# Kernel tuning notes

Measured on AMD Instinct MI355X. Metric: run time of the kernel, lower is better.

## Reference

```python
import jax, jax.numpy as jnp
import numpy as np

HEADS = 8


def setup_inputs() -> dict:
    key = jax.random.key(0)
    k0, k1, k2, k3 = jax.random.split(key, 4)
    N, C_in, T = 4, 256, 2048
    C_kq, C_out = 512, 512
    x = jax.random.normal(k0, (N, C_in, T), dtype=jnp.float32)
    # Conv1d(kernel_size=1, bias=False) weights squeezed to (out, in)
    Wq = jax.random.normal(k1, (C_kq, C_in), dtype=jnp.float32) * 0.02
    Wk = jax.random.normal(k2, (C_kq, C_in), dtype=jnp.float32) * 0.02
    Wv = jax.random.normal(k3, (C_out, C_in), dtype=jnp.float32) * 0.02
    return {"x": x, "Wq": Wq, "Wk": Wk, "Wv": Wv}


def reference(x, Wq, Wk, Wv):
    N, C, T = x.shape
    H = HEADS
    C_kq = Wq.shape[0]
    C_out = Wv.shape[0]
    dk = C_kq // H
    dv = C_out // H
    # 1x1 conv == per-timestep linear projection
    q = jnp.einsum('oc,nct->not', Wq, x).reshape(N, H, dk, T)
    k = jnp.einsum('oc,nct->not', Wk, x).reshape(N, H, dk, T)
    v = jnp.einsum('oc,nct->not', Wv, x).reshape(N, H, dv, T)
    scale = 1.0 / np.sqrt(dk)
    # scores[n,h,tk,tq] = sum_d q[n,h,d,tq] * k[n,h,d,tk]
    scores = jnp.einsum('nhdq,nhdk->nhkq', q, k) * scale
    attn = jax.nn.softmax(scores, axis=2)  # softmax over key axis tk
    # out[n,h,d,tq] = sum_tk attn[n,h,tk,tq] * v[n,h,d,tk]
    out = jnp.einsum('nhkq,nhdk->nhdq', attn, v)
    return out.reshape(N, C_out, T)
```

## Files before the change

### kernel.cpp

```cpp
#include <hip/hip_runtime.h>
#include <stdint.h>

#define T_SEQ 2048
#define CIN 256
#define COUT 512
#define NHEAD 8
#define DH 64
#define LROW 72

typedef __bf16 bf16x8 __attribute__((ext_vector_type(8)));
typedef float f32x4 __attribute__((ext_vector_type(4)));
typedef float f32x16 __attribute__((ext_vector_type(16)));
typedef unsigned short u16x8 __attribute__((ext_vector_type(8)));
typedef unsigned u32x4 __attribute__((ext_vector_type(4)));

static __device__ __forceinline__ unsigned short bf16_rne(float f) {
  unsigned u = __builtin_bit_cast(unsigned, f);
  u += 0x7FFFu + ((u >> 16) & 1u);
  return (unsigned short)(u >> 16);
}

static __device__ __forceinline__ unsigned cvt_pk_bf16(float lo, float hi) {
  unsigned r;
  asm("v_cvt_pk_bf16_f32 %0, %1, %2" : "=v"(r) : "v"(lo), "v"(hi));
  return r;
}

static __device__ __forceinline__ void plswap(unsigned& a, unsigned& b) {
  auto rr = __builtin_amdgcn_permlane32_swap((int)a, (int)b, false, false);
  a = (unsigned)rr[0];
  b = (unsigned)rr[1];
}

static __device__ __forceinline__ bf16x8 ld_frag(const unsigned short* p) {
  u16x8 v = *(const u16x8*)p;
  return __builtin_bit_cast(bf16x8, v);
}

__global__ __launch_bounds__(256) void pack_w_k(const float* __restrict__ wq,
                                                const float* __restrict__ wk,
                                                const float* __restrict__ wv,
                                                unsigned short* __restrict__ wb) {
  int i = blockIdx.x * 256 + threadIdx.x;
  const float* src = (i < 131072) ? wq : (i < 262144) ? wk : wv;
  wb[i] = bf16_rne(src[i & 131071]);
}

__global__ __launch_bounds__(256) void pack_xT_k(const float* __restrict__ x,
                                                 unsigned short* __restrict__ xT) {
  __shared__ float tile[64][65];
  const int n = blockIdx.z, c0 = blockIdx.y * 64, t0 = blockIdx.x * 64;
  const int i = threadIdx.x;
  {
    const int cc = i >> 2, tch = (i & 3) * 16;
    const float* src = x + ((size_t)n * CIN + c0 + cc) * T_SEQ + t0 + tch;
    const float4* s4 = (const float4*)src;
#pragma unroll
    for (int q = 0; q < 4; ++q) {
      float4 v = s4[q];
      tile[cc][tch + q * 4 + 0] = v.x;
      tile[cc][tch + q * 4 + 1] = v.y;
      tile[cc][tch + q * 4 + 2] = v.z;
      tile[cc][tch + q * 4 + 3] = v.w;
    }
  }
  __syncthreads();
  {
    const int tt = i >> 2, cch = (i & 3) * 16;
    unsigned short* dst = xT + ((size_t)n * T_SEQ + t0 + tt) * CIN + c0 + cch;
    u16x8 w0, w1;
#pragma unroll
    for (int j = 0; j < 8; ++j) w0[j] = bf16_rne(tile[cch + j][tt]);
#pragma unroll
    for (int j = 0; j < 8; ++j) w1[j] = bf16_rne(tile[cch + 8 + j][tt]);
    *(u16x8*)dst = w0;
    *(u16x8*)(dst + 8) = w1;
  }
}

__global__ __launch_bounds__(256) void proj_k(const unsigned short* __restrict__ wb,
                                              const unsigned short* __restrict__ xT,
                                              unsigned short* __restrict__ qb,
                                              unsigned short* __restrict__ kb,
                                              unsigned short* __restrict__ vb) {
  __shared__ unsigned short vt_lds[64][136];
  const int z = blockIdx.z;
  const int n = z / 3, w = z % 3;
  const unsigned short* W = wb + (size_t)w * COUT * CIN;
  const unsigned short* X = xT + (size_t)n * T_SEQ * CIN;
  const int tid = threadIdx.x, wave = tid >> 6, lane = tid & 63;
  const int c = lane & 15, g = lane >> 4;
  const int o0 = blockIdx.x * 64;
  const int t0 = blockIdx.y * 128 + wave * 32;

  f32x4 acc[2][4];
  const f32x4 z4 = {0.f, 0.f, 0.f, 0.f};
#pragma unroll
  for (int mt = 0; mt < 2; ++mt)
#pragma unroll
    for (int no = 0; no < 4; ++no) acc[mt][no] = z4;

  for (int c0 = 0; c0 < CIN; c0 += 32) {
    bf16x8 a[2], b[4];
#pragma unroll
    for (int mt = 0; mt < 2; ++mt)
      a[mt] = ld_frag(X + (size_t)(t0 + mt * 16 + c) * CIN + c0 + g * 8);
#pragma unroll
    for (int no = 0; no < 4; ++no)
      b[no] = ld_frag(W + (size_t)(o0 + no * 16 + c) * CIN + c0 + g * 8);
#pragma unroll
    for (int mt = 0; mt < 2; ++mt)
#pragma unroll
      for (int no = 0; no < 4; ++no)
        acc[mt][no] = __builtin_amdgcn_mfma_f32_16x16x32_bf16(a[mt], b[no], acc[mt][no], 0, 0, 0);
  }

  const int h = o0 >> 6;
  const size_t base = ((size_t)(n * NHEAD + h)) * T_SEQ * DH;
  if (w == 2) {
#pragma unroll
    for (int mt = 0; mt < 2; ++mt)
#pragma unroll
      for (int no = 0; no < 4; ++no) {
        const int d = no * 16 + c;
        const int lt = (wave * 32) + mt * 16 + 4 * g;
#pragma unroll
        for (int pr = 0; pr < 2; ++pr) {
          const unsigned pw = (unsigned)bf16_rne(acc[mt][no][2 * pr]) |
                              ((unsigned)bf16_rne(acc[mt][no][2 * pr + 1]) << 16);
          *(unsigned*)&vt_lds[d][lt + 2 * pr] = pw;
        }
      }
    __syncthreads();
    const int row = tid >> 2, seg = tid & 3;
    unsigned short* dst = vb + base + (size_t)row * T_SEQ + blockIdx.y * 128 + seg * 32;
    const unsigned short* srcl = &vt_lds[row][seg * 32];
#pragma unroll
    for (int q = 0; q < 4; ++q) *(u16x8*)(dst + q * 8) = *(const u16x8*)(srcl + q * 8);
  } else {
    unsigned short* dst = (w == 0) ? qb : kb;
    const float scale = (w == 0) ? 0.18033688011112043f : 1.0f;
#pragma unroll
    for (int mt = 0; mt < 2; ++mt)
#pragma unroll
      for (int no = 0; no < 4; ++no)
#pragma unroll
        for (int r = 0; r < 4; ++r) {
          const int t = t0 + mt * 16 + 4 * g + r;
          const int d = no * 16 + c;
          dst[base + (size_t)t * DH + d] = bf16_rne(acc[mt][no][r] * scale);
        }
  }
}

__global__ __launch_bounds__(512) void attn_k(const unsigned short* __restrict__ qb,
                                              const unsigned short* __restrict__ kb,
                                              const unsigned short* __restrict__ vbt,
                                              float* __restrict__ outp) {
  __shared__ unsigned short Kl[2][2][64 * LROW];
  __shared__ unsigned short Vt[2][2][64 * LROW];

  const int bid = blockIdx.x;
  const int sid = (bid & 7) * 64 + (bid >> 3);
  const int tqt = sid & 15, nh = sid >> 4;

  const int tid = threadIdx.x;
  const int wave = tid >> 6, lane = tid & 63;
  const int half = wave >> 2;
  const int ln = lane & 31, hi = lane >> 5;
  const int tq0 = tqt * 128 + (wave & 3) * 32;
  const unsigned short* Q = qb + (size_t)nh * T_SEQ * DH;
  const unsigned short* K = kb + (size_t)nh * T_SEQ * DH;
  const unsigned short* V = vbt + (size_t)nh * T_SEQ * DH;

  bf16x8 qf[4];
#pragma unroll
  for (int dblk = 0; dblk < 4; ++dblk)
    qf[dblk] = ld_frag(Q + (size_t)(tq0 + ln) * DH + dblk * 16 + hi * 8);

  const f32x16 z16 = {0.f, 0.f, 0.f, 0.f, 0.f, 0.f, 0.f, 0.f,
                      0.f, 0.f, 0.f, 0.f, 0.f, 0.f, 0.f, 0.f};
  f32x16 oacc0 = z16, oacc1 = z16;
  float l_run = 0.f;

  const int ht = tid & 255;
  const int srow = ht & 63, sseg = ht >> 6;
  const unsigned short* kseg = K + (size_t)(half * 1024 + srow) * DH + sseg * 16;
  const unsigned short* vseg = V + (size_t)srow * T_SEQ + half * 1024 + sseg * 16;
  const int swoff = srow * LROW + sseg * 16;
  const int row0 = ln * LROW;
  const int row1 = (32 + ln) * LROW;
  const int hioff = hi * 8;

  unsigned short* krb = &Kl[half][0][0];
  unsigned short* kab = &Kl[half][1][0];
  unsigned short* vrb = &Vt[half][0][0];
  unsigned short* vab = &Vt[half][1][0];
  {
    u16x8 k0 = *(const u16x8*)kseg;
    u16x8 k1 = *(const u16x8*)(kseg + 8);
    u16x8 v0 = *(const u16x8*)vseg;
    u16x8 v1 = *(const u16x8*)(vseg + 8);
    *(u16x8*)&krb[swoff] = k0;
    *(u16x8*)&krb[swoff + 8] = k1;
    *(u16x8*)&vrb[swoff] = v0;
    *(u16x8*)&vrb[swoff + 8] = v1;
  }
  __syncthreads();

  const int NT2 = T_SEQ / 64 / 2;
  for (int t = 0; t < NT2; ++t) {
    const bool pre = (t + 1 < NT2);
    u16x8 kn0, kn1, vn0, vn1;
    if (pre) {
      const unsigned short* ks = kseg + (size_t)(t + 1) * (64 * DH);
      kn0 = *(const u16x8*)ks;
      kn1 = *(const u16x8*)(ks + 8);
      const unsigned short* vs = vseg + (size_t)(t + 1) * 64;
      vn0 = *(const u16x8*)vs;
      vn1 = *(const u16x8*)(vs + 8);
    }
    f32x16 sa0 = z16, sa1 = z16;
    __builtin_amdgcn_s_setprio(1);
#pragma unroll
    for (int dblk = 0; dblk < 4; ++dblk) {
      bf16x8 ka0 = ld_frag(krb + row0 + dblk * 16 + hioff);
      bf16x8 ka1 = ld_frag(krb + row1 + dblk * 16 + hioff);
      sa0 = __builtin_amdgcn_mfma_f32_32x32x16_bf16(ka0, qf[dblk], sa0, 0, 0, 0);
      sa1 = __builtin_amdgcn_mfma_f32_32x32x16_bf16(ka1, qf[dblk], sa1, 0, 0, 0);
    }
    __builtin_amdgcn_s_setprio(0);
    float p0[16], p1[16];
    float cs = 0.f;
#pragma unroll
    for (int r = 0; r < 16; ++r) {
      p0[r] = __builtin_amdgcn_exp2f(sa0[r]);
      p1[r] = __builtin_amdgcn_exp2f(sa1[r]);
      cs += p0[r] + p1[r];
    }
    cs += __shfl_xor(cs, 32);
    l_run += cs;
    unsigned W0[8], W1[8];
#pragma unroll
    for (int j = 0; j < 8; ++j) {
      W0[j] = cvt_pk_bf16(p0[2 * j], p0[2 * j + 1]);
      W1[j] = cvt_pk_bf16(p1[2 * j], p1[2 * j + 1]);
    }
    plswap(W0[0], W0[2]);
    plswap(W0[1], W0[3]);
    plswap(W0[4], W0[6]);
    plswap(W0[5], W0[7]);
    plswap(W1[0], W1[2]);
    plswap(W1[1], W1[3]);
    plswap(W1[4], W1[6]);
    plswap(W1[5], W1[7]);
    bf16x8 pa[4];
    {
      u32x4 f;
      f[0] = W0[0]; f[1] = W0[1]; f[2] = W0[2]; f[3] = W0[3];
      pa[0] = __builtin_bit_cast(bf16x8, f);
      f[0] = W0[4]; f[1] = W0[5]; f[2] = W0[6]; f[3] = W0[7];
      pa[1] = __builtin_bit_cast(bf16x8, f);
      f[0] = W1[0]; f[1] = W1[1]; f[2] = W1[2]; f[3] = W1[3];
      pa[2] = __builtin_bit_cast(bf16x8, f);
      f[0] = W1[4]; f[1] = W1[5]; f[2] = W1[6]; f[3] = W1[7];
      pa[3] = __builtin_bit_cast(bf16x8, f);
    }
    __builtin_amdgcn_s_setprio(1);
#pragma unroll
    for (int kbk = 0; kbk < 4; ++kbk) {
      bf16x8 vf0 = ld_frag(vrb + row0 + kbk * 16 + hioff);
      bf16x8 vf1 = ld_frag(vrb + row1 + kbk * 16 + hioff);
      oacc0 = __builtin_amdgcn_mfma_f32_32x32x16_bf16(pa[kbk], vf0, oacc0, 0, 0, 0);
      oacc1 = __builtin_amdgcn_mfma_f32_32x32x16_bf16(pa[kbk], vf1, oacc1, 0, 0, 0);
    }
    __builtin_amdgcn_s_setprio(0);
    if (pre) {
      *(u16x8*)&kab[swoff] = kn0;
      *(u16x8*)&kab[swoff + 8] = kn1;
      *(u16x8*)&vab[swoff] = vn0;
      *(u16x8*)&vab[swoff + 8] = vn1;
    }
    __syncthreads();
    unsigned short* tp;
    tp = krb; krb = kab; kab = tp;
    tp = vrb; vrb = vab; vab = tp;
  }

  float* mbuf = (float*)&Kl[0][0][0];
  const int MS = 2112;
  if (half == 1) {
    float* mb = mbuf + (wave - 4) * MS;
#pragma unroll
    for (int r = 0; r < 16; ++r) mb[r * 64 + lane] = oacc0[r];
#pragma unroll
    for (int r = 0; r < 16; ++r) mb[1024 + r * 64 + lane] = oacc1[r];
    mb[2048 + lane] = l_run;
  }
  __syncthreads();
  if (half == 0) {
    float* mb = mbuf + wave * MS;
#pragma unroll
    for (int r = 0; r < 16; ++r) oacc0[r] += mb[r * 64 + lane];
#pragma unroll
    for (int r = 0; r < 16; ++r) oacc1[r] += mb[1024 + r * 64 + lane];
    l_run += mb[2048 + lane];

    const int n = nh >> 3, h = nh & 7;
    const size_t obase = (size_t)(n * COUT + h * DH) * T_SEQ;
    const int d0 = ln, d1 = 32 + ln;
#pragma unroll
    for (int rq = 0; rq < 4; ++rq) {
      const int tbase = tq0 + 8 * rq + 4 * hi;
      f32x4 o0, o1;
#pragma unroll
      for (int j = 0; j < 4; ++j) {
        const float lv = __shfl(l_run, 8 * rq + 4 * hi + j);
        const float inv = __builtin_amdgcn_rcpf(lv);
        o0[j] = oacc0[4 * rq + j] * inv;
        o1[j] = oacc1[4 * rq + j] * inv;
      }
      *(f32x4*)&outp[obase + (size_t)d0 * T_SEQ + tbase] = o0;
      *(f32x4*)&outp[obase + (size_t)d1 * T_SEQ + tbase] = o1;
    }
  }
}

extern "C" void kernel_launch(void* const* d_in, const int* in_sizes, int n_in,
                              void* d_out, int out_size, void* d_ws, size_t ws_size,
                              hipStream_t stream) {
  (void)in_sizes; (void)n_in; (void)out_size; (void)ws_size;
  const float* x  = (const float*)d_in[0];
  const float* Wq = (const float*)d_in[1];
  const float* Wk = (const float*)d_in[2];
  const float* Wv = (const float*)d_in[3];
  float* outp = (float*)d_out;

  char* ws = (char*)d_ws;
  unsigned short* wb = (unsigned short*)ws;
  unsigned short* xT = (unsigned short*)(ws + 786432);
  unsigned short* qb = (unsigned short*)(ws + 4980736);
  unsigned short* kb = qb + 4194304;
  unsigned short* vb = kb + 4194304;

  pack_w_k<<<1536, 256, 0, stream>>>(Wq, Wk, Wv, wb);
  pack_xT_k<<<dim3(32, 4, 4), 256, 0, stream>>>(x, xT);
  proj_k<<<dim3(8, 16, 12), 256, 0, stream>>>(wb, xT, qb, kb, vb);
  attn_k<<<512, 512, 0, stream>>>(qb, kb, vb, outp);
}
```

Before: 105.5 us.

## Ping-pong QK and softmax/PV phases between the two wave halves

Splits each loop iteration into two barrier-separated phases and staggers the halves: while one half runs the QK MFMAs, the other runs exp/softmax and the PV MFMAs on the previous tile. Half 1's PV lags by one tile and is finished after the loop. The goal is to overlap the matrix-core work of one wave group with the transcendental/VALU work of the other. The cost is an extra __syncthreads per iteration and scores held in registers across the barrier, which may add register pressure.

```diff
diff --git a/kernel.cpp b/kernel.cpp
--- a/kernel.cpp
+++ b/kernel.cpp
@@ -192,50 +192,26 @@
   const int row1 = (32 + ln) * LROW;
   const int hioff = hi * 8;
 
-  unsigned short* krb = &Kl[half][0][0];
-  unsigned short* kab = &Kl[half][1][0];
-  unsigned short* vrb = &Vt[half][0][0];
-  unsigned short* vab = &Vt[half][1][0];
-  {
-    u16x8 k0 = *(const u16x8*)kseg;
-    u16x8 k1 = *(const u16x8*)(kseg + 8);
-    u16x8 v0 = *(const u16x8*)vseg;
-    u16x8 v1 = *(const u16x8*)(vseg + 8);
-    *(u16x8*)&krb[swoff] = k0;
-    *(u16x8*)&krb[swoff + 8] = k1;
-    *(u16x8*)&vrb[swoff] = v0;
-    *(u16x8*)&vrb[swoff + 8] = v1;
-  }
-  __syncthreads();
-
-  const int NT2 = T_SEQ / 64 / 2;
-  for (int t = 0; t < NT2; ++t) {
-    const bool pre = (t + 1 < NT2);
-    u16x8 kn0, kn1, vn0, vn1;
-    if (pre) {
-      const unsigned short* ks = kseg + (size_t)(t + 1) * (64 * DH);
-      kn0 = *(const u16x8*)ks;
-      kn1 = *(const u16x8*)(ks + 8);
-      const unsigned short* vs = vseg + (size_t)(t + 1) * 64;
-      vn0 = *(const u16x8*)vs;
-      vn1 = *(const u16x8*)(vs + 8);
-    }
-    f32x16 sa0 = z16, sa1 = z16;
+  auto qk = [&](const unsigned short* kbp, f32x16& s0, f32x16& s1) {
+    s0 = z16;
+    s1 = z16;
     __builtin_amdgcn_s_setprio(1);
 #pragma unroll
     for (int dblk = 0; dblk < 4; ++dblk) {
-      bf16x8 ka0 = ld_frag(krb + row0 + dblk * 16 + hioff);
-      bf16x8 ka1 = ld_frag(krb + row1 + dblk * 16 + hioff);
-      sa0 = __builtin_amdgcn_mfma_f32_32x32x16_bf16(ka0, qf[dblk], sa0, 0, 0, 0);
-      sa1 = __builtin_amdgcn_mfma_f32_32x32x16_bf16(ka1, qf[dblk], sa1, 0, 0, 0);
+      bf16x8 ka0 = ld_frag(kbp + row0 + dblk * 16 + hioff);
+      bf16x8 ka1 = ld_frag(kbp + row1 + dblk * 16 + hioff);
+      s0 = __builtin_amdgcn_mfma_f32_32x32x16_bf16(ka0, qf[dblk], s0, 0, 0, 0);
+      s1 = __builtin_amdgcn_mfma_f32_32x32x16_bf16(ka1, qf[dblk], s1, 0, 0, 0);
     }
     __builtin_amdgcn_s_setprio(0);
+  };
+  auto smpv = [&](const f32x16& s0, const f32x16& s1, const unsigned short* vbp) {
     float p0[16], p1[16];
     float cs = 0.f;
 #pragma unroll
     for (int r = 0; r < 16; ++r) {
-      p0[r] = __builtin_amdgcn_exp2f(sa0[r]);
-      p1[r] = __builtin_amdgcn_exp2f(sa1[r]);
+      p0[r] = __builtin_amdgcn_exp2f(s0[r]);
+      p1[r] = __builtin_amdgcn_exp2f(s1[r]);
       cs += p0[r] + p1[r];
     }
     cs += __shfl_xor(cs, 32);
@@ -269,12 +245,54 @@
     __builtin_amdgcn_s_setprio(1);
 #pragma unroll
     for (int kbk = 0; kbk < 4; ++kbk) {
-      bf16x8 vf0 = ld_frag(vrb + row0 + kbk * 16 + hioff);
-      bf16x8 vf1 = ld_frag(vrb + row1 + kbk * 16 + hioff);
+      bf16x8 vf0 = ld_frag(vbp + row0 + kbk * 16 + hioff);
+      bf16x8 vf1 = ld_frag(vbp + row1 + kbk * 16 + hioff);
       oacc0 = __builtin_amdgcn_mfma_f32_32x32x16_bf16(pa[kbk], vf0, oacc0, 0, 0, 0);
       oacc1 = __builtin_amdgcn_mfma_f32_32x32x16_bf16(pa[kbk], vf1, oacc1, 0, 0, 0);
     }
     __builtin_amdgcn_s_setprio(0);
+  };
+
+  unsigned short* krb = &Kl[half][0][0];
+  unsigned short* kab = &Kl[half][1][0];
+  unsigned short* vrb = &Vt[half][0][0];
+  unsigned short* vab = &Vt[half][1][0];
+  {
+    u16x8 k0 = *(const u16x8*)kseg;
+    u16x8 k1 = *(const u16x8*)(kseg + 8);
+    u16x8 v0 = *(const u16x8*)vseg;
+    u16x8 v1 = *(const u16x8*)(vseg + 8);
+    *(u16x8*)&krb[swoff] = k0;
+    *(u16x8*)&krb[swoff + 8] = k1;
+    *(u16x8*)&vrb[swoff] = v0;
+    *(u16x8*)&vrb[swoff + 8] = v1;
+  }
+  __syncthreads();
+
+  f32x16 sa0, sa1;
+  const int NT2 = T_SEQ / 64 / 2;
+  for (int t = 0; t < NT2; ++t) {
+    const bool pre = (t + 1 < NT2);
+    u16x8 kn0, kn1, vn0, vn1;
+    if (pre) {
+      const unsigned short* ks = kseg + (size_t)(t + 1) * (64 * DH);
+      kn0 = *(const u16x8*)ks;
+      kn1 = *(const u16x8*)(ks + 8);
+      const unsigned short* vs = vseg + (size_t)(t + 1) * 64;
+      vn0 = *(const u16x8*)vs;
+      vn1 = *(const u16x8*)(vs + 8);
+    }
+    if (half == 0) {
+      qk(krb, sa0, sa1);
+    } else if (t > 0) {
+      smpv(sa0, sa1, vab);
+    }
+    __syncthreads();
+    if (half == 0) {
+      smpv(sa0, sa1, vrb);
+    } else {
+      qk(krb, sa0, sa1);
+    }
     if (pre) {
       *(u16x8*)&kab[swoff] = kn0;
       *(u16x8*)&kab[swoff + 8] = kn1;
@@ -286,6 +304,7 @@
     tp = krb; krb = kab; kab = tp;
     tp = vrb; vrb = vab; vab = tp;
   }
+  if (half == 1) smpv(sa0, sa1, vab);
 
   float* mbuf = (float*)&Kl[0][0][0];
   const int MS = 2112;
```

Result: slower. 113.2 us (+7.3%).

## Fuse QKV projections per block and drop split-K attention for smaller blocks

Applied to the files above, without the earlier changes.

The projection kernel now loads the X fragments once into registers and loops over the three weight matrices (Q, K, V) inside one block, cutting grid z from 12 to 4 and reusing activations. The attention kernel drops the two-half key split and its LDS merge, using 128-thread blocks of 64 queries that walk all 32 key tiles, launched as 1024 blocks. This removes the cross-half reduction and halves LDS per block. In exchange each wave runs a longer serial key loop, and proj_k holds more registers for the cached fragments.

```diff
diff --git a/kernel.cpp b/kernel.cpp
--- a/kernel.cpp
+++ b/kernel.cpp
@@ -84,91 +84,97 @@
                                               unsigned short* __restrict__ kb,
                                               unsigned short* __restrict__ vb) {
   __shared__ unsigned short vt_lds[64][136];
-  const int z = blockIdx.z;
-  const int n = z / 3, w = z % 3;
-  const unsigned short* W = wb + (size_t)w * COUT * CIN;
+  const int n = blockIdx.z;
   const unsigned short* X = xT + (size_t)n * T_SEQ * CIN;
   const int tid = threadIdx.x, wave = tid >> 6, lane = tid & 63;
   const int c = lane & 15, g = lane >> 4;
   const int o0 = blockIdx.x * 64;
   const int t0 = blockIdx.y * 128 + wave * 32;
 
-  f32x4 acc[2][4];
+  bf16x8 a[8][2];
+#pragma unroll
+  for (int k8 = 0; k8 < 8; ++k8)
+#pragma unroll
+    for (int mt = 0; mt < 2; ++mt)
+      a[k8][mt] = ld_frag(X + (size_t)(t0 + mt * 16 + c) * CIN + k8 * 32 + g * 8);
+
   const f32x4 z4 = {0.f, 0.f, 0.f, 0.f};
-#pragma unroll
-  for (int mt = 0; mt < 2; ++mt)
-#pragma unroll
-    for (int no = 0; no < 4; ++no) acc[mt][no] = z4;
-
-  for (int c0 = 0; c0 < CIN; c0 += 32) {
-    bf16x8 a[2], b[4];
-#pragma unroll
-    for (int mt = 0; mt < 2; ++mt)
-      a[mt] = ld_frag(X + (size_t)(t0 + mt * 16 + c) * CIN + c0 + g * 8);
-#pragma unroll
-    for (int no = 0; no < 4; ++no)
-      b[no] = ld_frag(W + (size_t)(o0 + no * 16 + c) * CIN + c0 + g * 8);
-#pragma unroll
-    for (int mt = 0; mt < 2; ++mt)
-#pragma unroll
-      for (int no = 0; no < 4; ++no)
-        acc[mt][no] = __builtin_amdgcn_mfma_f32_16x16x32_bf16(a[mt], b[no], acc[mt][no], 0, 0, 0);
-  }
-
   const int h = o0 >> 6;
   const size_t base = ((size_t)(n * NHEAD + h)) * T_SEQ * DH;
-  if (w == 2) {
+
+  for (int w = 0; w < 3; ++w) {
+    const unsigned short* W = wb + (size_t)w * COUT * CIN;
+    f32x4 acc[2][4];
 #pragma unroll
     for (int mt = 0; mt < 2; ++mt)
 #pragma unroll
-      for (int no = 0; no < 4; ++no) {
-        const int d = no * 16 + c;
-        const int lt = (wave * 32) + mt * 16 + 4 * g;
-#pragma unroll
-        for (int pr = 0; pr < 2; ++pr) {
-          const unsigned pw = (unsigned)bf16_rne(acc[mt][no][2 * pr]) |
-                              ((unsigned)bf16_rne(acc[mt][no][2 * pr + 1]) << 16);
-          *(unsigned*)&vt_lds[d][lt + 2 * pr] = pw;
+      for (int no = 0; no < 4; ++no) acc[mt][no] = z4;
+
+#pragma unroll
+    for (int k8 = 0; k8 < 8; ++k8) {
+      bf16x8 b[4];
+#pragma unroll
+      for (int no = 0; no < 4; ++no)
+        b[no] = ld_frag(W + (size_t)(o0 + no * 16 + c) * CIN + k8 * 32 + g * 8);
+#pragma unroll
+      for (int mt = 0; mt < 2; ++mt)
+#pragma unroll
+        for (int no = 0; no < 4; ++no)
+          acc[mt][no] = __builtin_amdgcn_mfma_f32_16x16x32_bf16(a[k8][mt], b[no], acc[mt][no], 0, 0, 0);
+    }
+
+    if (w == 2) {
+#pragma unroll
+      for (int mt = 0; mt < 2; ++mt)
+#pragma unroll
+        for (int no = 0; no < 4; ++no) {
+          const int d = no * 16 + c;
+          const int lt = (wave * 32) + mt * 16 + 4 * g;
+#pragma unroll
+          for (int pr = 0; pr < 2; ++pr) {
+            const unsigned pw = (unsigned)bf16_rne(acc[mt][no][2 * pr]) |
+                                ((unsigned)bf16_rne(acc[mt][no][2 * pr + 1]) << 16);
+            *(unsigned*)&vt_lds[d][lt + 2 * pr] = pw;
+          }
         }
-      }
-    __syncthreads();
-    const int row = tid >> 2, seg = tid & 3;
-    unsigned short* dst = vb + base + (size_t)row * T_SEQ + blockIdx.y * 128 + seg * 32;
-    const unsigned short* srcl = &vt_lds[row][seg * 32];
-#pragma unroll
-    for (int q = 0; q < 4; ++q) *(u16x8*)(dst + q * 8) = *(const u16x8*)(srcl + q * 8);
-  } else {
-    unsigned short* dst = (w == 0) ? qb : kb;
-    const float scale = (w == 0) ? 0.18033688011112043f : 1.0f;
-#pragma unroll
-    for (int mt = 0; mt < 2; ++mt)
-#pragma unroll
-      for (int no = 0; no < 4; ++no)
-#pragma unroll
-        for (int r = 0; r < 4; ++r) {
-          const int t = t0 + mt * 16 + 4 * g + r;
-          const int d = no * 16 + c;
-          dst[base + (size_t)t * DH + d] = bf16_rne(acc[mt][no][r] * scale);
-        }
-  }
-}
-
-__global__ __launch_bounds__(512) void attn_k(const unsigned short* __restrict__ qb,
+      __syncthreads();
+      const int row = tid >> 2, seg = tid & 3;
+      unsigned short* dst = vb + base + (size_t)row * T_SEQ + blockIdx.y * 128 + seg * 32;
+      const unsigned short* srcl = &vt_lds[row][seg * 32];
+#pragma unroll
+      for (int q = 0; q < 4; ++q) *(u16x8*)(dst + q * 8) = *(const u16x8*)(srcl + q * 8);
+    } else {
+      unsigned short* dst = (w == 0) ? qb : kb;
+      const float scale = (w == 0) ? 0.18033688011112043f : 1.0f;
+#pragma unroll
+      for (int mt = 0; mt < 2; ++mt)
+#pragma unroll
+        for (int no = 0; no < 4; ++no)
+#pragma unroll
+          for (int r = 0; r < 4; ++r) {
+            const int t = t0 + mt * 16 + 4 * g + r;
+            const int d = no * 16 + c;
+            dst[base + (size_t)t * DH + d] = bf16_rne(acc[mt][no][r] * scale);
+          }
+    }
+  }
+}
+
+__global__ __launch_bounds__(128) void attn_k(const unsigned short* __restrict__ qb,
                                               const unsigned short* __restrict__ kb,
                                               const unsigned short* __restrict__ vbt,
                                               float* __restrict__ outp) {
-  __shared__ unsigned short Kl[2][2][64 * LROW];
-  __shared__ unsigned short Vt[2][2][64 * LROW];
+  __shared__ unsigned short Kl[2][64 * LROW];
+  __shared__ unsigned short Vt[2][64 * LROW];
 
   const int bid = blockIdx.x;
-  const int sid = (bid & 7) * 64 + (bid >> 3);
-  const int tqt = sid & 15, nh = sid >> 4;
+  const int sid = (bid & 7) * 128 + (bid >> 3);
+  const int tqt = sid & 31, nh = sid >> 5;
 
   const int tid = threadIdx.x;
   const int wave = tid >> 6, lane = tid & 63;
-  const int half = wave >> 2;
   const int ln = lane & 31, hi = lane >> 5;
-  const int tq0 = tqt * 128 + (wave & 3) * 32;
+  const int tq0 = tqt * 64 + wave * 32;
   const unsigned short* Q = qb + (size_t)nh * T_SEQ * DH;
   const unsigned short* K = kb + (size_t)nh * T_SEQ * DH;
   const unsigned short* V = vbt + (size_t)nh * T_SEQ * DH;
@@ -183,42 +189,50 @@
   f32x16 oacc0 = z16, oacc1 = z16;
   float l_run = 0.f;
 
-  const int ht = tid & 255;
-  const int srow = ht & 63, sseg = ht >> 6;
-  const unsigned short* kseg = K + (size_t)(half * 1024 + srow) * DH + sseg * 16;
-  const unsigned short* vseg = V + (size_t)srow * T_SEQ + half * 1024 + sseg * 16;
-  const int swoff = srow * LROW + sseg * 16;
+  const int srow = tid & 63, shalf = tid >> 6;
+  const unsigned short* kseg = K + (size_t)srow * DH + shalf * 32;
+  const unsigned short* vseg = V + (size_t)srow * T_SEQ + shalf * 32;
+  const int swoff = srow * LROW + shalf * 32;
   const int row0 = ln * LROW;
   const int row1 = (32 + ln) * LROW;
   const int hioff = hi * 8;
 
-  unsigned short* krb = &Kl[half][0][0];
-  unsigned short* kab = &Kl[half][1][0];
-  unsigned short* vrb = &Vt[half][0][0];
-  unsigned short* vab = &Vt[half][1][0];
+  unsigned short* krb = &Kl[0][0];
+  unsigned short* kab = &Kl[1][0];
+  unsigned short* vrb = &Vt[0][0];
+  unsigned short* vab = &Vt[1][0];
   {
     u16x8 k0 = *(const u16x8*)kseg;
     u16x8 k1 = *(const u16x8*)(kseg + 8);
+    u16x8 k2 = *(const u16x8*)(kseg + 16);
+    u16x8 k3 = *(const u16x8*)(kseg + 24);
     u16x8 v0 = *(const u16x8*)vseg;
     u16x8 v1 = *(const u16x8*)(vseg + 8);
+    u16x8 v2 = *(const u16x8*)(vseg + 16);
+    u16x8 v3 = *(const u16x8*)(vseg + 24);
     *(u16x8*)&krb[swoff] = k0;
     *(u16x8*)&krb[swoff + 8] = k1;
+    *(u16x8*)&krb[swoff + 16] = k2;
+    *(u16x8*)&krb[swoff + 24] = k3;
     *(u16x8*)&vrb[swoff] = v0;
     *(u16x8*)&vrb[swoff + 8] = v1;
+    *(u16x8*)&vrb[swoff + 16] = v2;
+    *(u16x8*)&vrb[swoff + 24] = v3;
   }
   __syncthreads();
 
-  const int NT2 = T_SEQ / 64 / 2;
-  for (int t = 0; t < NT2; ++t) {
-    const bool pre = (t + 1 < NT2);
-    u16x8 kn0, kn1, vn0, vn1;
+  const int NT = T_SEQ / 64;
+  for (int t = 0; t < NT; ++t) {
+    const bool pre = (t + 1 < NT);
+    u16x8 kn[4], vn[4];
     if (pre) {
       const unsigned short* ks = kseg + (size_t)(t + 1) * (64 * DH);
-      kn0 = *(const u16x8*)ks;
-      kn1 = *(const u16x8*)(ks + 8);
       const unsigned short* vs = vseg + (size_t)(t + 1) * 64;
-      vn0 = *(const u16x8*)vs;
-      vn1 = *(const u16x8*)(vs + 8);
+#pragma unroll
+      for (int j = 0; j < 4; ++j) {
+        kn[j] = *(const u16x8*)(ks + j * 8);
+        vn[j] = *(const u16x8*)(vs + j * 8);
+      }
     }
     f32x16 sa0 = z16, sa1 = z16;
     __builtin_amdgcn_s_setprio(1);
@@ -276,10 +290,11 @@
     }
     __builtin_amdgcn_s_setprio(0);
     if (pre) {
-      *(u16x8*)&kab[swoff] = kn0;
-      *(u16x8*)&kab[swoff + 8] = kn1;
-      *(u16x8*)&vab[swoff] = vn0;
-      *(u16x8*)&vab[swoff + 8] = vn1;
+#pragma unroll
+      for (int j = 0; j < 4; ++j) {
+        *(u16x8*)&kab[swoff + j * 8] = kn[j];
+        *(u16x8*)&vab[swoff + j * 8] = vn[j];
+      }
     }
     __syncthreads();
     unsigned short* tp;
@@ -287,42 +302,22 @@
     tp = vrb; vrb = vab; vab = tp;
   }
 
-  float* mbuf = (float*)&Kl[0][0][0];
-  const int MS = 2112;
-  if (half == 1) {
-    float* mb = mbuf + (wave - 4) * MS;
-#pragma unroll
-    for (int r = 0; r < 16; ++r) mb[r * 64 + lane] = oacc0[r];
-#pragma unroll
-    for (int r = 0; r < 16; ++r) mb[1024 + r * 64 + lane] = oacc1[r];
-    mb[2048 + lane] = l_run;
-  }
-  __syncthreads();
-  if (half == 0) {
-    float* mb = mbuf + wave * MS;
-#pragma unroll
-    for (int r = 0; r < 16; ++r) oacc0[r] += mb[r * 64 + lane];
-#pragma unroll
-    for (int r = 0; r < 16; ++r) oacc1[r] += mb[1024 + r * 64 + lane];
-    l_run += mb[2048 + lane];
-
-    const int n = nh >> 3, h = nh & 7;
-    const size_t obase = (size_t)(n * COUT + h * DH) * T_SEQ;
-    const int d0 = ln, d1 = 32 + ln;
-#pragma unroll
-    for (int rq = 0; rq < 4; ++rq) {
-      const int tbase = tq0 + 8 * rq + 4 * hi;
-      f32x4 o0, o1;
-#pragma unroll
-      for (int j = 0; j < 4; ++j) {
-        const float lv = __shfl(l_run, 8 * rq + 4 * hi + j);
-        const float inv = __builtin_amdgcn_rcpf(lv);
-        o0[j] = oacc0[4 * rq + j] * inv;
-        o1[j] = oacc1[4 * rq + j] * inv;
-      }
-      *(f32x4*)&outp[obase + (size_t)d0 * T_SEQ + tbase] = o0;
-      *(f32x4*)&outp[obase + (size_t)d1 * T_SEQ + tbase] = o1;
-    }
+  const int n = nh >> 3, h = nh & 7;
+  const size_t obase = (size_t)(n * COUT + h * DH) * T_SEQ;
+  const int d0 = ln, d1 = 32 + ln;
+#pragma unroll
+  for (int rq = 0; rq < 4; ++rq) {
+    const int tbase = tq0 + 8 * rq + 4 * hi;
+    f32x4 o0, o1;
+#pragma unroll
+    for (int j = 0; j < 4; ++j) {
+      const float lv = __shfl(l_run, 8 * rq + 4 * hi + j);
+      const float inv = __builtin_amdgcn_rcpf(lv);
+      o0[j] = oacc0[4 * rq + j] * inv;
+      o1[j] = oacc1[4 * rq + j] * inv;
+    }
+    *(f32x4*)&outp[obase + (size_t)d0 * T_SEQ + tbase] = o0;
+    *(f32x4*)&outp[obase + (size_t)d1 * T_SEQ + tbase] = o1;
   }
 }
 
@@ -345,6 +340,6 @@
 
   pack_w_k<<<1536, 256, 0, stream>>>(Wq, Wk, Wv, wb);
   pack_xT_k<<<dim3(32, 4, 4), 256, 0, stream>>>(x, xT);
-  proj_k<<<dim3(8, 16, 12), 256, 0, stream>>>(wb, xT, qb, kb, vb);
-  attn_k<<<512, 512, 0, stream>>>(qb, kb, vb, outp);
-}
+  proj_k<<<dim3(8, 16, 4), 256, 0, stream>>>(wb, xT, qb, kb, vb);
+  attn_k<<<1024, 128, 0, stream>>>(qb, kb, vb, outp);
+}
```

New measurement: 112.1 us. 1.06x slower.

## Double per-wave query tile in attention and fuse QKV projections per block

Applied to the files above, without the earlier changes.

The attention kernel now has each wave handle 64 queries instead of 32. Every K/V fragment read from LDS feeds twice as many MFMAs, and the grid drops to 256 blocks. The projection kernel keeps x fragments in registers and loops over the three weight matrices inside one block instead of launching a separate block per matrix. The aim is less LDS and global reload traffic per FLOP, at the cost of higher register pressure (four 32x32 accumulators, a larger x-fragment cache) and fewer blocks to fill the GPU.

```diff
diff --git a/kernel.cpp b/kernel.cpp
--- a/kernel.cpp
+++ b/kernel.cpp
@@ -84,72 +84,79 @@
                                               unsigned short* __restrict__ kb,
                                               unsigned short* __restrict__ vb) {
   __shared__ unsigned short vt_lds[64][136];
-  const int z = blockIdx.z;
-  const int n = z / 3, w = z % 3;
-  const unsigned short* W = wb + (size_t)w * COUT * CIN;
+  const int n = blockIdx.z;
   const unsigned short* X = xT + (size_t)n * T_SEQ * CIN;
   const int tid = threadIdx.x, wave = tid >> 6, lane = tid & 63;
   const int c = lane & 15, g = lane >> 4;
   const int o0 = blockIdx.x * 64;
   const int t0 = blockIdx.y * 128 + wave * 32;
 
-  f32x4 acc[2][4];
+  bf16x8 a[8][2];
+#pragma unroll
+  for (int k8 = 0; k8 < 8; ++k8)
+#pragma unroll
+    for (int mt = 0; mt < 2; ++mt)
+      a[k8][mt] = ld_frag(X + (size_t)(t0 + mt * 16 + c) * CIN + k8 * 32 + g * 8);
+
   const f32x4 z4 = {0.f, 0.f, 0.f, 0.f};
-#pragma unroll
-  for (int mt = 0; mt < 2; ++mt)
-#pragma unroll
-    for (int no = 0; no < 4; ++no) acc[mt][no] = z4;
-
-  for (int c0 = 0; c0 < CIN; c0 += 32) {
-    bf16x8 a[2], b[4];
-#pragma unroll
-    for (int mt = 0; mt < 2; ++mt)
-      a[mt] = ld_frag(X + (size_t)(t0 + mt * 16 + c) * CIN + c0 + g * 8);
-#pragma unroll
-    for (int no = 0; no < 4; ++no)
-      b[no] = ld_frag(W + (size_t)(o0 + no * 16 + c) * CIN + c0 + g * 8);
-#pragma unroll
-    for (int mt = 0; mt < 2; ++mt)
-#pragma unroll
-      for (int no = 0; no < 4; ++no)
-        acc[mt][no] = __builtin_amdgcn_mfma_f32_16x16x32_bf16(a[mt], b[no], acc[mt][no], 0, 0, 0);
-  }
-
   const int h = o0 >> 6;
   const size_t base = ((size_t)(n * NHEAD + h)) * T_SEQ * DH;
-  if (w == 2) {
+
+  for (int w = 0; w < 3; ++w) {
+    const unsigned short* W = wb + (size_t)w * COUT * CIN;
+    f32x4 acc[2][4];
 #pragma unroll
     for (int mt = 0; mt < 2; ++mt)
 #pragma unroll
-      for (int no = 0; no < 4; ++no) {
-        const int d = no * 16 + c;
-        const int lt = (wave * 32) + mt * 16 + 4 * g;
-#pragma unroll
-        for (int pr = 0; pr < 2; ++pr) {
-          const unsigned pw = (unsigned)bf16_rne(acc[mt][no][2 * pr]) |
-                              ((unsigned)bf16_rne(acc[mt][no][2 * pr + 1]) << 16);
-          *(unsigned*)&vt_lds[d][lt + 2 * pr] = pw;
+      for (int no = 0; no < 4; ++no) acc[mt][no] = z4;
+
+#pragma unroll
+    for (int k8 = 0; k8 < 8; ++k8) {
+      bf16x8 b[4];
+#pragma unroll
+      for (int no = 0; no < 4; ++no)
+        b[no] = ld_frag(W + (size_t)(o0 + no * 16 + c) * CIN + k8 * 32 + g * 8);
+#pragma unroll
+      for (int mt = 0; mt < 2; ++mt)
+#pragma unroll
+        for (int no = 0; no < 4; ++no)
+          acc[mt][no] = __builtin_amdgcn_mfma_f32_16x16x32_bf16(a[k8][mt], b[no], acc[mt][no], 0, 0, 0);
+    }
+
+    if (w == 2) {
+#pragma unroll
+      for (int mt = 0; mt < 2; ++mt)
+#pragma unroll
+        for (int no = 0; no < 4; ++no) {
+          const int d = no * 16 + c;
+          const int lt = (wave * 32) + mt * 16 + 4 * g;
+#pragma unroll
+          for (int pr = 0; pr < 2; ++pr) {
+            const unsigned pw = (unsigned)bf16_rne(acc[mt][no][2 * pr]) |
+                                ((unsigned)bf16_rne(acc[mt][no][2 * pr + 1]) << 16);
+            *(unsigned*)&vt_lds[d][lt + 2 * pr] = pw;
+          }
         }
-      }
-    __syncthreads();
-    const int row = tid >> 2, seg = tid & 3;
-    unsigned short* dst = vb + base + (size_t)row * T_SEQ + blockIdx.y * 128 + seg * 32;
-    const unsigned short* srcl = &vt_lds[row][seg * 32];
-#pragma unroll
-    for (int q = 0; q < 4; ++q) *(u16x8*)(dst + q * 8) = *(const u16x8*)(srcl + q * 8);
-  } else {
-    unsigned short* dst = (w == 0) ? qb : kb;
-    const float scale = (w == 0) ? 0.18033688011112043f : 1.0f;
-#pragma unroll
-    for (int mt = 0; mt < 2; ++mt)
-#pragma unroll
-      for (int no = 0; no < 4; ++no)
-#pragma unroll
-        for (int r = 0; r < 4; ++r) {
-          const int t = t0 + mt * 16 + 4 * g + r;
-          const int d = no * 16 + c;
-          dst[base + (size_t)t * DH + d] = bf16_rne(acc[mt][no][r] * scale);
-        }
+      __syncthreads();
+      const int row = tid >> 2, seg = tid & 3;
+      unsigned short* dst = vb + base + (size_t)row * T_SEQ + blockIdx.y * 128 + seg * 32;
+      const unsigned short* srcl = &vt_lds[row][seg * 32];
+#pragma unroll
+      for (int q = 0; q < 4; ++q) *(u16x8*)(dst + q * 8) = *(const u16x8*)(srcl + q * 8);
+    } else {
+      unsigned short* dst = (w == 0) ? qb : kb;
+      const float scale = (w == 0) ? 0.18033688011112043f : 1.0f;
+#pragma unroll
+      for (int mt = 0; mt < 2; ++mt)
+#pragma unroll
+        for (int no = 0; no < 4; ++no)
+#pragma unroll
+          for (int r = 0; r < 4; ++r) {
+            const int t = t0 + mt * 16 + 4 * g + r;
+            const int d = no * 16 + c;
+            dst[base + (size_t)t * DH + d] = bf16_rne(acc[mt][no][r] * scale);
+          }
+    }
   }
 }
 
@@ -157,31 +164,33 @@
                                               const unsigned short* __restrict__ kb,
                                               const unsigned short* __restrict__ vbt,
                                               float* __restrict__ outp) {
-  __shared__ unsigned short Kl[2][2][64 * LROW];
-  __shared__ unsigned short Vt[2][2][64 * LROW];
+  __shared__ unsigned short smem[4 * 2 * 4608];
 
   const int bid = blockIdx.x;
-  const int sid = (bid & 7) * 64 + (bid >> 3);
-  const int tqt = sid & 15, nh = sid >> 4;
+  const int sid = (bid & 7) * 32 + (bid >> 3);
+  const int tqt = sid & 7, nh = sid >> 3;
 
   const int tid = threadIdx.x;
   const int wave = tid >> 6, lane = tid & 63;
   const int half = wave >> 2;
   const int ln = lane & 31, hi = lane >> 5;
-  const int tq0 = tqt * 128 + (wave & 3) * 32;
+  const int tq0 = tqt * 256 + (wave & 3) * 64;
   const unsigned short* Q = qb + (size_t)nh * T_SEQ * DH;
   const unsigned short* K = kb + (size_t)nh * T_SEQ * DH;
   const unsigned short* V = vbt + (size_t)nh * T_SEQ * DH;
 
-  bf16x8 qf[4];
-#pragma unroll
-  for (int dblk = 0; dblk < 4; ++dblk)
-    qf[dblk] = ld_frag(Q + (size_t)(tq0 + ln) * DH + dblk * 16 + hi * 8);
+  bf16x8 qf0[4], qf1[4];
+#pragma unroll
+  for (int dblk = 0; dblk < 4; ++dblk) {
+    qf0[dblk] = ld_frag(Q + (size_t)(tq0 + ln) * DH + dblk * 16 + hi * 8);
+    qf1[dblk] = ld_frag(Q + (size_t)(tq0 + 32 + ln) * DH + dblk * 16 + hi * 8);
+  }
 
   const f32x16 z16 = {0.f, 0.f, 0.f, 0.f, 0.f, 0.f, 0.f, 0.f,
                       0.f, 0.f, 0.f, 0.f, 0.f, 0.f, 0.f, 0.f};
-  f32x16 oacc0 = z16, oacc1 = z16;
-  float l_run = 0.f;
+  f32x16 oacc00 = z16, oacc01 = z16;
+  f32x16 oacc10 = z16, oacc11 = z16;
+  float l_run0 = 0.f, l_run1 = 0.f;
 
   const int ht = tid & 255;
   const int srow = ht & 63, sseg = ht >> 6;
@@ -192,10 +201,10 @@
   const int row1 = (32 + ln) * LROW;
   const int hioff = hi * 8;
 
-  unsigned short* krb = &Kl[half][0][0];
-  unsigned short* kab = &Kl[half][1][0];
-  unsigned short* vrb = &Vt[half][0][0];
-  unsigned short* vab = &Vt[half][1][0];
+  unsigned short* krb = smem + half * 18432;
+  unsigned short* kab = krb + 4608;
+  unsigned short* vrb = krb + 9216;
+  unsigned short* vab = krb + 13824;
   {
     u16x8 k0 = *(const u16x8*)kseg;
     u16x8 k1 = *(const u16x8*)(kseg + 8);
@@ -220,59 +229,90 @@
       vn0 = *(const u16x8*)vs;
       vn1 = *(const u16x8*)(vs + 8);
     }
-    f32x16 sa0 = z16, sa1 = z16;
+    f32x16 sa00 = z16, sa01 = z16, sa10 = z16, sa11 = z16;
     __builtin_amdgcn_s_setprio(1);
 #pragma unroll
     for (int dblk = 0; dblk < 4; ++dblk) {
       bf16x8 ka0 = ld_frag(krb + row0 + dblk * 16 + hioff);
       bf16x8 ka1 = ld_frag(krb + row1 + dblk * 16 + hioff);
-      sa0 = __builtin_amdgcn_mfma_f32_32x32x16_bf16(ka0, qf[dblk], sa0, 0, 0, 0);
-      sa1 = __builtin_amdgcn_mfma_f32_32x32x16_bf16(ka1, qf[dblk], sa1, 0, 0, 0);
+      sa00 = __builtin_amdgcn_mfma_f32_32x32x16_bf16(ka0, qf0[dblk], sa00, 0, 0, 0);
+      sa01 = __builtin_amdgcn_mfma_f32_32x32x16_bf16(ka1, qf0[dblk], sa01, 0, 0, 0);
+      sa10 = __builtin_amdgcn_mfma_f32_32x32x16_bf16(ka0, qf1[dblk], sa10, 0, 0, 0);
+      sa11 = __builtin_amdgcn_mfma_f32_32x32x16_bf16(ka1, qf1[dblk], sa11, 0, 0, 0);
     }
     __builtin_amdgcn_s_setprio(0);
-    float p0[16], p1[16];
-    float cs = 0.f;
-#pragma unroll
-    for (int r = 0; r < 16; ++r) {
-      p0[r] = __builtin_amdgcn_exp2f(sa0[r]);
-      p1[r] = __builtin_amdgcn_exp2f(sa1[r]);
-      cs += p0[r] + p1[r];
-    }
-    cs += __shfl_xor(cs, 32);
-    l_run += cs;
-    unsigned W0[8], W1[8];
-#pragma unroll
-    for (int j = 0; j < 8; ++j) {
-      W0[j] = cvt_pk_bf16(p0[2 * j], p0[2 * j + 1]);
-      W1[j] = cvt_pk_bf16(p1[2 * j], p1[2 * j + 1]);
-    }
-    plswap(W0[0], W0[2]);
-    plswap(W0[1], W0[3]);
-    plswap(W0[4], W0[6]);
-    plswap(W0[5], W0[7]);
-    plswap(W1[0], W1[2]);
-    plswap(W1[1], W1[3]);
-    plswap(W1[4], W1[6]);
-    plswap(W1[5], W1[7]);
-    bf16x8 pa[4];
+    bf16x8 pa0[4], pa1[4];
     {
+      float p0[16], p1[16];
+      float cs = 0.f;
+#pragma unroll
+      for (int r = 0; r < 16; ++r) {
+        p0[r] = __builtin_amdgcn_exp2f(sa00[r]);
+        p1[r] = __builtin_amdgcn_exp2f(sa01[r]);
+        cs += p0[r] + p1[r];
+      }
+      cs += __shfl_xor(cs, 32);
+      l_run0 += cs;
+      unsigned W0[8], W1[8];
+#pragma unroll
+      for (int j = 0; j < 8; ++j) {
+        W0[j] = cvt_pk_bf16(p0[2 * j], p0[2 * j + 1]);
+        W1[j] = cvt_pk_bf16(p1[2 * j], p1[2 * j + 1]);
+      }
+      plswap(W0[0], W0[2]); plswap(W0[1], W0[3]);
+      plswap(W0[4], W0[6]); plswap(W0[5], W0[7]);
+      plswap(W1[0], W1[2]); plswap(W1[1], W1[3]);
+      plswap(W1[4], W1[6]); plswap(W1[5], W1[7]);
       u32x4 f;
       f[0] = W0[0]; f[1] = W0[1]; f[2] = W0[2]; f[3] = W0[3];
-      pa[0] = __builtin_bit_cast(bf16x8, f);
+      pa0[0] = __builtin_bit_cast(bf16x8, f);
       f[0] = W0[4]; f[1] = W0[5]; f[2] = W0[6]; f[3] = W0[7];
-      pa[1] = __builtin_bit_cast(bf16x8, f);
+      pa0[1] = __builtin_bit_cast(bf16x8, f);
       f[0] = W1[0]; f[1] = W1[1]; f[2] = W1[2]; f[3] = W1[3];
-      pa[2] = __builtin_bit_cast(bf16x8, f);
+      pa0[2] = __builtin_bit_cast(bf16x8, f);
       f[0] = W1[4]; f[1] = W1[5]; f[2] = W1[6]; f[3] = W1[7];
-      pa[3] = __builtin_bit_cast(bf16x8, f);
+      pa0[3] = __builtin_bit_cast(bf16x8, f);
+    }
+    {
+      float p0[16], p1[16];
+      float cs = 0.f;
+#pragma unroll
+      for (int r = 0; r < 16; ++r) {
+        p0[r] = __builtin_amdgcn_exp2f(sa10[r]);
+        p1[r] = __builtin_amdgcn_exp2f(sa11[r]);
+        cs += p0[r] + p1[r];
+      }
+      cs += __shfl_xor(cs, 32);
+      l_run1 += cs;
+      unsigned W0[8], W1[8];
+#pragma unroll
+      for (int j = 0; j < 8; ++j) {
+        W0[j] = cvt_pk_bf16(p0[2 * j], p0[2 * j + 1]);
+        W1[j] = cvt_pk_bf16(p1[2 * j], p1[2 * j + 1]);
+      }
+      plswap(W0[0], W0[2]); plswap(W0[1], W0[3]);
+      plswap(W0[4], W0[6]); plswap(W0[5], W0[7]);
+      plswap(W1[0], W1[2]); plswap(W1[1], W1[3]);
+      plswap(W1[4], W1[6]); plswap(W1[5], W1[7]);
+      u32x4 f;
+      f[0] = W0[0]; f[1] = W0[1]; f[2] = W0[2]; f[3] = W0[3];
+      pa1[0] = __builtin_bit_cast(bf16x8, f);
+      f[0] = W0[4]; f[1] = W0[5]; f[2] = W0[6]; f[3] = W0[7];
+      pa1[1] = __builtin_bit_cast(bf16x8, f);
+      f[0] = W1[0]; f[1] = W1[1]; f[2] = W1[2]; f[3] = W1[3];
+      pa1[2] = __builtin_bit_cast(bf16x8, f);
+      f[0] = W1[4]; f[1] = W1[5]; f[2] = W1[6]; f[3] = W1[7];
+      pa1[3] = __builtin_bit_cast(bf16x8, f);
     }
     __builtin_amdgcn_s_setprio(1);
 #pragma unroll
     for (int kbk = 0; kbk < 4; ++kbk) {
       bf16x8 vf0 = ld_frag(vrb + row0 + kbk * 16 + hioff);
       bf16x8 vf1 = ld_frag(vrb + row1 + kbk * 16 + hioff);
-      oacc0 = __builtin_amdgcn_mfma_f32_32x32x16_bf16(pa[kbk], vf0, oacc0, 0, 0, 0);
-      oacc1 = __builtin_amdgcn_mfma_f32_32x32x16_bf16(pa[kbk], vf1, oacc1, 0, 0, 0);
+      oacc00 = __builtin_amdgcn_mfma_f32_32x32x16_bf16(pa0[kbk], vf0, oacc00, 0, 0, 0);
+      oacc01 = __builtin_amdgcn_mfma_f32_32x32x16_bf16(pa0[kbk], vf1, oacc01, 0, 0, 0);
+      oacc10 = __builtin_amdgcn_mfma_f32_32x32x16_bf16(pa1[kbk], vf0, oacc10, 0, 0, 0);
+      oacc11 = __builtin_amdgcn_mfma_f32_32x32x16_bf16(pa1[kbk], vf1, oacc11, 0, 0, 0);
     }
     __builtin_amdgcn_s_setprio(0);
     if (pre) {
@@ -287,24 +327,34 @@
     tp = vrb; vrb = vab; vab = tp;
   }
 
-  float* mbuf = (float*)&Kl[0][0][0];
-  const int MS = 2112;
+  float* mbuf = (float*)smem;
+  const int MS = 4224;
   if (half == 1) {
     float* mb = mbuf + (wave - 4) * MS;
 #pragma unroll
-    for (int r = 0; r < 16; ++r) mb[r * 64 + lane] = oacc0[r];
-#pragma unroll
-    for (int r = 0; r < 16; ++r) mb[1024 + r * 64 + lane] = oacc1[r];
-    mb[2048 + lane] = l_run;
+    for (int r = 0; r < 16; ++r) mb[r * 64 + lane] = oacc00[r];
+#pragma unroll
+    for (int r = 0; r < 16; ++r) mb[1024 + r * 64 + lane] = oacc01[r];
+#pragma unroll
+    for (int r = 0; r < 16; ++r) mb[2048 + r * 64 + lane] = oacc10[r];
+#pragma unroll
+    for (int r = 0; r < 16; ++r) mb[3072 + r * 64 + lane] = oacc11[r];
+    mb[4096 + lane] = l_run0;
+    mb[4160 + lane] = l_run1;
   }
   __syncthreads();
   if (half == 0) {
     float* mb = mbuf + wave * MS;
 #pragma unroll
-    for (int r = 0; r < 16; ++r) oacc0[r] += mb[r * 64 + lane];
-#pragma unroll
-    for (int r = 0; r < 16; ++r) oacc1[r] += mb[1024 + r * 64 + lane];
-    l_run += mb[2048 + lane];
+    for (int r = 0; r < 16; ++r) oacc00[r] += mb[r * 64 + lane];
+#pragma unroll
+    for (int r = 0; r < 16; ++r) oacc01[r] += mb[1024 + r * 64 + lane];
+#pragma unroll
+    for (int r = 0; r < 16; ++r) oacc10[r] += mb[2048 + r * 64 + lane];
+#pragma unroll
+    for (int r = 0; r < 16; ++r) oacc11[r] += mb[3072 + r * 64 + lane];
+    l_run0 += mb[4096 + lane];
+    l_run1 += mb[4160 + lane];
 
     const int n = nh >> 3, h = nh & 7;
     const size_t obase = (size_t)(n * COUT + h * DH) * T_SEQ;
@@ -312,16 +362,22 @@
 #pragma unroll
     for (int rq = 0; rq < 4; ++rq) {
       const int tbase = tq0 + 8 * rq + 4 * hi;
-      f32x4 o0, o1;
+      f32x4 o0, o1, o2, o3;
 #pragma unroll
       for (int j = 0; j < 4; ++j) {
-        const float lv = __shfl(l_run, 8 * rq + 4 * hi + j);
-        const float inv = __builtin_amdgcn_rcpf(lv);
-        o0[j] = oacc0[4 * rq + j] * inv;
-        o1[j] = oacc1[4 * rq + j] * inv;
+        const float lv0 = __shfl(l_run0, 8 * rq + 4 * hi + j);
+        const float inv0 = __builtin_amdgcn_rcpf(lv0);
+        const float lv1 = __shfl(l_run1, 8 * rq + 4 * hi + j);
+        const float inv1 = __builtin_amdgcn_rcpf(lv1);
+        o0[j] = oacc00[4 * rq + j] * inv0;
+        o1[j] = oacc01[4 * rq + j] * inv0;
+        o2[j] = oacc10[4 * rq + j] * inv1;
+        o3[j] = oacc11[4 * rq + j] * inv1;
       }
       *(f32x4*)&outp[obase + (size_t)d0 * T_SEQ + tbase] = o0;
       *(f32x4*)&outp[obase + (size_t)d1 * T_SEQ + tbase] = o1;
+      *(f32x4*)&outp[obase + (size_t)d0 * T_SEQ + tbase + 32] = o2;
+      *(f32x4*)&outp[obase + (size_t)d1 * T_SEQ + tbase + 32] = o3;
     }
   }
 }
@@ -345,6 +401,6 @@
 
   pack_w_k<<<1536, 256, 0, stream>>>(Wq, Wk, Wv, wb);
   pack_xT_k<<<dim3(32, 4, 4), 256, 0, stream>>>(x, xT);
-  proj_k<<<dim3(8, 16, 12), 256, 0, stream>>>(wb, xT, qb, kb, vb);
-  attn_k<<<512, 512, 0, stream>>>(qb, kb, vb, outp);
-}
+  proj_k<<<dim3(8, 16, 4), 256, 0, stream>>>(wb, xT, qb, kb, vb);
+  attn_k<<<256, 512, 0, stream>>>(qb, kb, vb, outp);
+}
```

After: 87.22 us. -17.3%, faster.
